# Kernel tuning notes

Measured on AMD Instinct MI355X. Metric: run time of the kernel, lower is better.

Reference implementation:

```python
import jax, jax.numpy as jnp
import numpy as np

EMBED_DIM = 1024
NUM_HEADS = 16
HEAD_DIM = EMBED_DIM // NUM_HEADS


def setup_inputs() -> dict:
    key = jax.random.key(0)
    ks = jax.random.split(key, 11)
    B, S, D = 2, 2048, EMBED_DIM
    s = 1.0 / np.sqrt(D)
    inp = {
        "query": jax.random.normal(ks[0], (B, S, D), jnp.float32),
        "key": jax.random.normal(ks[1], (B, S, D), jnp.float32),
        "value": jax.random.normal(ks[2], (B, S, D), jnp.float32),
        # torch Linear weights: [out, in]
        "Wq": jax.random.normal(ks[3], (D, D), jnp.float32) * s,
        "bq": jnp.zeros((D,), jnp.float32),
        "Wk": jax.random.normal(ks[4], (D, D), jnp.float32) * s,
        "bk": jnp.zeros((D,), jnp.float32),
        "Wv": jax.random.normal(ks[5], (D, D), jnp.float32) * s,
        "bv": jnp.zeros((D,), jnp.float32),
        "Wo": jax.random.normal(ks[6], (D, D), jnp.float32) * s,
        "bo": jnp.zeros((D,), jnp.float32),
    }
    return inp


def reference(query, key, value, Wq, bq, Wk, bk, Wv, bv, Wo, bo):
    B, Q, D = query.shape
    K = key.shape[1]
    H, Hd = NUM_HEADS, HEAD_DIM
    # NOTE: source divides by scaling = head_dim**-0.5, i.e. multiplies by sqrt(head_dim)
    scaling = float(Hd) ** (-0.5)

    q = (query @ Wq.T + bq).reshape(B, Q, H, Hd).transpose(0, 2, 1, 3)  # [B,H,Q,Hd]
    k = (key @ Wk.T + bk).reshape(B, K, H, Hd).transpose(0, 2, 1, 3)    # [B,H,K,Hd]
    v = (value @ Wv.T + bv).reshape(B, K, H, Hd).transpose(0, 2, 1, 3)  # [B,H,K,Hd]

    scores = jnp.einsum("bhqd,bhkd->bhqk", q, k) / scaling
    attn = jax.nn.softmax(scores, axis=-1)  # dropout=0 (eval)
    out = jnp.einsum("bhqk,bhkd->bhqd", attn, v)
    out = out.transpose(0, 2, 1, 3).reshape(B, Q, D)
    return out @ Wo.T + bo
```

## Files before the change

kernel.cpp:

```cpp
#include <hip/hip_runtime.h>
#include <type_traits>
#include <utility>

#define B_ 2
#define S_ 2048
#define D_ 1024
#define H_ 16
#define HD_ 64
#define KDIM 1024

typedef __attribute__((ext_vector_type(8))) short    s16x8;
typedef __attribute__((ext_vector_type(8))) _Float16 h16x8;
typedef __attribute__((ext_vector_type(4))) float    f32x4;
typedef __attribute__((ext_vector_type(4))) int      i32x4;
typedef __attribute__((ext_vector_type(2))) int      i32x2;

template <typename T, typename = void> struct mfma_takes : std::false_type {};
template <typename T>
struct mfma_takes<T, std::void_t<decltype(__builtin_amdgcn_mfma_f32_16x16x32_f16(
    std::declval<T>(), std::declval<T>(), std::declval<f32x4>(), 0, 0, 0))>>
    : std::true_type {};
using frag8 = std::conditional_t<mfma_takes<h16x8>::value, h16x8, s16x8>;

__device__ __forceinline__ f32x4 mfma_f16(frag8 a, frag8 b, f32x4 c) {
  return __builtin_amdgcn_mfma_f32_16x16x32_f16(a, b, c, 0, 0, 0);
}

__device__ __forceinline__ short f2h(float f) {
  _Float16 h = (_Float16)f;
  short s; __builtin_memcpy(&s, &h, 2);
  return s;
}
__device__ __forceinline__ int pk2h(float a, float b) {
  auto p = __builtin_amdgcn_cvt_pkrtz(a, b);
  int r; __builtin_memcpy(&r, &p, 4); return r;
}
__device__ __forceinline__ frag8 ld_frag(const short* p) {
  return __builtin_bit_cast(frag8, *(const i32x4*)p);
}
__device__ __forceinline__ float fast_exp2(float x) {
  return __builtin_amdgcn_exp2f(x);
}

typedef __attribute__((address_space(1))) const void gvoid;
typedef __attribute__((address_space(3))) void lvoid;
__device__ __forceinline__ void async_copy16(const void* g, void* l) {
  __builtin_amdgcn_global_load_lds((gvoid*)g, (lvoid*)l, 16, 0, 0);
}

#define RAW_BARRIER() asm volatile("s_barrier" ::: "memory")
#define WAITCNT_VM(n) asm volatile("s_waitcnt vmcnt(" #n ")" ::: "memory")

__global__ __launch_bounds__(256)
void conv_all(const float* __restrict__ q, const float* __restrict__ k,
              const float* __restrict__ v, const float* __restrict__ Wq,
              const float* __restrict__ Wk, const float* __restrict__ Wv,
              const float* __restrict__ Wo,
              short* __restrict__ qh, short* __restrict__ kh,
              short* __restrict__ vh, short* __restrict__ wq,
              short* __restrict__ wk, short* __restrict__ wv,
              short* __restrict__ wo) {
  const int blk = blockIdx.x;
  const float* src; short* dst; int base;
  if (blk < 2048)      { src = q;  dst = qh; base = blk; }
  else if (blk < 4096) { src = k;  dst = kh; base = blk - 2048; }
  else if (blk < 6144) { src = v;  dst = vh; base = blk - 4096; }
  else if (blk < 6656) { src = Wq; dst = wq; base = blk - 6144; }
  else if (blk < 7168) { src = Wk; dst = wk; base = blk - 6656; }
  else if (blk < 7680) { src = Wv; dst = wv; base = blk - 7168; }
  else                 { src = Wo; dst = wo; base = blk - 7680; }
  const int i = base * 2048 + threadIdx.x * 8;
  float4 a0 = *(const float4*)(src + i);
  float4 a1 = *(const float4*)(src + i + 4);
  short h[8] = { f2h(a0.x), f2h(a0.y), f2h(a0.z), f2h(a0.w),
                 f2h(a1.x), f2h(a1.y), f2h(a1.z), f2h(a1.w) };
  i32x4 ph; __builtin_memcpy(&ph, h, 16);
  *(i32x4*)(dst + i) = ph;
}

__global__ __launch_bounds__(256, 3)
void gemm_qkv(const short* __restrict__ qh, const short* __restrict__ kh,
              const short* __restrict__ vh, const short* __restrict__ wq,
              const short* __restrict__ wk, const short* __restrict__ wv,
              const float* __restrict__ bq, const float* __restrict__ bk,
              const float* __restrict__ bv, short* __restrict__ Qf,
              short* __restrict__ Kf, short* __restrict__ Vt, float QS) {
  __shared__ short As[3 * 4096];
  __shared__ short Bs[3 * 4096];

  const int blk = blockIdx.x;
  const int xcd = blk & 7, i = blk >> 3;
  const int p = (i >> 3) * 8 + xcd;
  const int bn = i & 7;
  const int z = p >> 5, bm = p & 31;
  const short* Ap = z == 0 ? qh : z == 1 ? kh : vh;
  const short* Wp = z == 0 ? wq : z == 1 ? wk : wv;
  const float* bias = z == 0 ? bq : z == 1 ? bk : bv;
  short* Out = z == 0 ? Qf : z == 1 ? Kf : Vt;
  const float scale = z == 0 ? QS : 1.0f;
  const int omode = z == 2 ? 2 : 1;

  const int t = threadIdx.x, wave = t >> 6, lane = t & 63;
  const int laneN = lane & 15, quad = lane >> 4;
  const int wm = wave & 1, wn = wave >> 1;

  f32x4 acc[4][4];
#pragma unroll
  for (int i2 = 0; i2 < 4; ++i2)
#pragma unroll
    for (int j = 0; j < 4; ++j)
#pragma unroll
      for (int r = 0; r < 4; ++r) acc[i2][j][r] = 0.f;

  auto stage = [&](int buf, int kk) {
#pragma unroll
    for (int j = 0; j < 2; ++j) {
      const int chunk = j * 256 + t;
      const int row = chunk >> 2;
      const int gg = (chunk & 3) ^ ((row >> 1) & 3);
      async_copy16(Ap + (size_t)(bm * 128 + row) * KDIM + kk + gg * 8,
                   As + buf * 4096 + chunk * 8);
      async_copy16(Wp + (size_t)(bn * 128 + row) * KDIM + kk + gg * 8,
                   Bs + buf * 4096 + chunk * 8);
    }
  };

  stage(0, 0);
  stage(1, 32);
  int buf = 0;
  for (int kk = 0; kk < KDIM; kk += 32) {
    if (kk + 64 < KDIM) {
      int nb = buf + 2; if (nb >= 3) nb -= 3;
      stage(nb, kk + 64);
      WAITCNT_VM(8);
    } else if (kk + 32 < KDIM) {
      WAITCNT_VM(4);
    } else {
      WAITCNT_VM(0);
    }
    RAW_BARRIER();

    frag8 aF[4], bF[4];
#pragma unroll
    for (int mi = 0; mi < 4; ++mi) {
      const int row = wm * 64 + mi * 16 + laneN;
      aF[mi] = ld_frag(As + buf * 4096 + row * 32 +
                       ((quad ^ ((row >> 1) & 3)) * 8));
    }
#pragma unroll
    for (int ni = 0; ni < 4; ++ni) {
      const int row = wn * 64 + ni * 16 + laneN;
      bF[ni] = ld_frag(Bs + buf * 4096 + row * 32 +
                       ((quad ^ ((row >> 1) & 3)) * 8));
    }
#pragma unroll
    for (int mi = 0; mi < 4; ++mi)
#pragma unroll
      for (int ni = 0; ni < 4; ++ni)
        acc[mi][ni] = mfma_f16(aF[mi], bF[ni], acc[mi][ni]);
    RAW_BARRIER();
    buf = buf + 1 == 3 ? 0 : buf + 1;
  }

  short* scr = As + wave * 1152;
  const int h = bn * 2 + wn;
  if (omode == 2) {
    const int bidx = bm >> 4;
    const int sbase = (bm * 128 + wm * 64) & 2047;
#pragma unroll
    for (int ni = 0; ni < 4; ++ni) {
      const float bb = bias[bn * 128 + wn * 64 + ni * 16 + laneN];
#pragma unroll
      for (int mi = 0; mi < 4; ++mi) {
        short pk[4];
#pragma unroll
        for (int r = 0; r < 4; ++r) pk[r] = f2h(acc[mi][ni][r] + bb);
        i32x2 w; __builtin_memcpy(&w, pk, 8);
        *(i32x2*)(scr + laneN * 72 + mi * 16 + quad * 4) = w;
      }
#pragma unroll
      for (int j = 0; j < 2; ++j) {
        const int ff = lane * 2 + j, hdr = ff >> 3, ch = ff & 7;
        i32x4 v = *(const i32x4*)(scr + hdr * 72 + ch * 8);
        *(i32x4*)(Vt + (((size_t)(bidx * H_ + h)) * HD_ + ni * 16 + hdr) * S_ +
                  sbase + ch * 8) = v;
      }
    }
  } else {
#pragma unroll
    for (int mi = 0; mi < 4; ++mi) {
#pragma unroll
      for (int ni = 0; ni < 4; ++ni) {
        const float bb = bias[bn * 128 + wn * 64 + ni * 16 + laneN];
#pragma unroll
        for (int r = 0; r < 4; ++r)
          scr[(quad * 4 + r) * 72 + ni * 16 + laneN] =
              f2h((acc[mi][ni][r] + bb) * scale);
      }
#pragma unroll
      for (int j = 0; j < 2; ++j) {
        const int ff = lane * 2 + j, row = ff >> 3, ch = ff & 7;
        const int rowg = bm * 128 + wm * 64 + mi * 16 + row;
        const int bidx = rowg >> 11, s = rowg & 2047;
        i32x4 v = *(const i32x4*)(scr + row * 72 + ch * 8);
        *(i32x4*)(Out + (((size_t)(bidx * H_ + h)) * S_ + s) * HD_ + ch * 8) = v;
      }
    }
  }
}

__global__ __launch_bounds__(256, 3)
void gemm_out(const short* __restrict__ Ap, const short* __restrict__ Wp,
              const float* __restrict__ bias, float* __restrict__ Out) {
  __shared__ short As[2 * 8192];
  __shared__ short Bs[2 * 4096];
  const int blk = blockIdx.x;
  const int xcd = blk & 7, i = blk >> 3;
  const int bm = (i >> 4) * 8 + xcd;
  const int bn = i & 15;

  const int t = threadIdx.x, wave = t >> 6, lane = t & 63;
  const int laneN = lane & 15, quad = lane >> 4;
  const int wm = wave & 1, wn = wave >> 1;

  f32x4 acc[4][2];
#pragma unroll
  for (int i2 = 0; i2 < 4; ++i2)
#pragma unroll
    for (int j = 0; j < 2; ++j)
#pragma unroll
      for (int r = 0; r < 4; ++r) acc[i2][j][r] = 0.f;

  auto stage = [&](int buf, int kk) {
#pragma unroll
    for (int j = 0; j < 4; ++j) {
      const int c = j * 256 + t;
      const int row = c >> 3, g = (c & 7) ^ (row & 7);
      async_copy16(Ap + (size_t)(bm * 128 + row) * KDIM + kk + g * 8,
                   As + buf * 8192 + c * 8);
    }
#pragma unroll
    for (int j = 0; j < 2; ++j) {
      const int c = j * 256 + t;
      const int row = c >> 3, g = (c & 7) ^ (row & 7);
      async_copy16(Wp + (size_t)(bn * 64 + row) * KDIM + kk + g * 8,
                   Bs + buf * 4096 + c * 8);
    }
  };

  int offA[4][2], offB[2][2];
#pragma unroll
  for (int mi = 0; mi < 4; ++mi) {
    const int row = wm * 64 + mi * 16 + laneN;
#pragma unroll
    for (int ks = 0; ks < 2; ++ks)
      offA[mi][ks] = row * 64 + (((quad + 4 * ks) ^ (row & 7)) * 8);
  }
#pragma unroll
  for (int ni = 0; ni < 2; ++ni) {
    const int row = wn * 32 + ni * 16 + laneN;
#pragma unroll
    for (int ks = 0; ks < 2; ++ks)
      offB[ni][ks] = row * 64 + (((quad + 4 * ks) ^ (row & 7)) * 8);
  }

  stage(0, 0);
  int buf = 0;
  for (int kk = 0; kk < KDIM; kk += 64) {
    if (kk + 64 < KDIM) {
      stage(buf ^ 1, kk + 64);
      WAITCNT_VM(6);
    } else {
      WAITCNT_VM(0);
    }
    RAW_BARRIER();

    frag8 aF[4][2], bF[2][2];
#pragma unroll
    for (int mi = 0; mi < 4; ++mi) {
      aF[mi][0] = ld_frag(As + buf * 8192 + offA[mi][0]);
      aF[mi][1] = ld_frag(As + buf * 8192 + offA[mi][1]);
    }
#pragma unroll
    for (int ni = 0; ni < 2; ++ni) {
      bF[ni][0] = ld_frag(Bs + buf * 4096 + offB[ni][0]);
      bF[ni][1] = ld_frag(Bs + buf * 4096 + offB[ni][1]);
    }
#pragma unroll
    for (int mi = 0; mi < 4; ++mi)
#pragma unroll
      for (int ni = 0; ni < 2; ++ni) {
        acc[mi][ni] = mfma_f16(aF[mi][0], bF[ni][0], acc[mi][ni]);
        acc[mi][ni] = mfma_f16(aF[mi][1], bF[ni][1], acc[mi][ni]);
      }
    RAW_BARRIER();
    buf ^= 1;
  }

  float* scr = (float*)As + wave * 576;
#pragma unroll
  for (int mi = 0; mi < 4; ++mi) {
#pragma unroll
    for (int ni = 0; ni < 2; ++ni) {
      const float bb = bias[bn * 64 + wn * 32 + ni * 16 + laneN];
#pragma unroll
      for (int r = 0; r < 4; ++r)
        scr[(quad * 4 + r) * 36 + ni * 16 + laneN] = acc[mi][ni][r] + bb;
    }
#pragma unroll
    for (int j = 0; j < 2; ++j) {
      const int ff = lane * 2 + j, row = ff >> 3, ch = ff & 7;
      const int rowg = bm * 128 + wm * 64 + mi * 16 + row;
      f32x4 v = *(const f32x4*)(scr + row * 36 + ch * 4);
      *(f32x4*)(Out + (size_t)rowg * 1024 + bn * 64 + wn * 32 + ch * 4) = v;
    }
  }
}

__global__ __launch_bounds__(512, 4)
void attn(const short* __restrict__ Qf, const short* __restrict__ Kf,
          const short* __restrict__ Vt_, short* __restrict__ Ow) {
  __shared__ short Ks[4 * 4096];
  __shared__ short Vts[4 * 4096];
  __shared__ short Ps[8][16 * 64];

  const int blk = blockIdx.x;
  const int xcd = blk & 7, local = blk >> 3;
  const int pair = xcd * 4 + (local >> 4);
  const int h = pair & 15, b = pair >> 4, qt = local & 15;
  const size_t head = ((size_t)b * H_ + h) * (size_t)S_ * HD_;

  const int t = threadIdx.x;
  const int wave = t >> 6, lane = t & 63;
  const int laneN = lane & 15, quad = lane >> 4;

  frag8 qf[2];
  {
    const size_t row = (size_t)qt * 128 + wave * 16 + laneN;
#pragma unroll
    for (int half = 0; half < 2; ++half)
      qf[half] = ld_frag(Qf + head + row * HD_ + half * 32 + quad * 8);
  }

  f32x4 o[4];
  float m_r = -1e30f, l_r = 0.f;
#pragma unroll
  for (int i = 0; i < 4; ++i)
#pragma unroll
    for (int j = 0; j < 4; ++j) o[i][j] = 0.f;

  const int srow = t >> 3, sg = (t & 7) ^ (srow & 7);
  const short* kp = Kf + head + (size_t)srow * HD_ + sg * 8;
  const short* vp = Vt_ + head + (size_t)srow * S_ + sg * 8;
  const int d = t * 8;

  int off[4][2];
#pragma unroll
  for (int nt = 0; nt < 4; ++nt) {
    const int row = nt * 16 + laneN;
    off[nt][0] = row * 64 + ((quad ^ (row & 7)) * 8);
    off[nt][1] = row * 64 + (((quad + 4) ^ (row & 7)) * 8);
  }

  short* const pwr = &Ps[wave][0] + laneN * 64;
  short* pw[4];
#pragma unroll
  for (int nt = 0; nt < 4; ++nt) {
    const int g = nt * 2 + (quad >> 1);
    pw[nt] = pwr + ((g + laneN) & 7) * 8 + (quad & 1) * 4;
  }
  const short* prd0 = pwr + ((quad + laneN) & 7) * 8;
  const short* prd1 = pwr + (((quad + 4) + laneN) & 7) * 8;

  async_copy16(kp, Ks + d);  async_copy16(vp, Vts + d);
  kp += 4096; vp += 64;
  async_copy16(kp, Ks + 4096 + d);  async_copy16(vp, Vts + 4096 + d);
  kp += 4096; vp += 64;

  f32x4 s[4];
  WAITCNT_VM(2);
  RAW_BARRIER();
  {
    __builtin_amdgcn_s_setprio(1);
#pragma unroll
    for (int nt = 0; nt < 4; ++nt) {
      frag8 k0 = ld_frag(Ks + off[nt][0]);
      frag8 k1 = ld_frag(Ks + off[nt][1]);
      f32x4 acc = {0.f, 0.f, 0.f, 0.f};
      acc = mfma_f16(k0, qf[0], acc);
      acc = mfma_f16(k1, qf[1], acc);
      s[nt] = acc;
    }
    __builtin_amdgcn_s_setprio(0);
  }

#define ATTN_TILE(B0, STG, QKN)                                              \
  {                                                                          \
    if (STG == 1) {                                                          \
      async_copy16(kp, Ks + (((B0) + 2) & 3) * 4096 + d);                    \
      async_copy16(vp, Vts + (((B0) + 2) & 3) * 4096 + d);                   \
      kp += 4096; vp += 64;                                                  \
      WAITCNT_VM(2);                                                         \
    } else if (STG == 2) {                                                   \
      WAITCNT_VM(0);                                                         \
    }                                                                        \
    RAW_BARRIER();                                                           \
    const short* VbS = Vts + (B0) * 4096;                                    \
                              \
    frag8 vf[4][2];                                                          \
    _Pragma("unroll")                                                        \
    for (int dt = 0; dt < 4; ++dt) {                                         \
      vf[dt][0] = ld_frag(VbS + off[dt][0]);                                 \
      vf[dt][1] = ld_frag(VbS + off[dt][1]);                                 \
    }                                                                        \
                         \
    f32x4 sn[4];                                                             \
    if (QKN) {                                                               \
      const short* KbS = Ks + (((B0) + 1) & 3) * 4096;                       \
      __builtin_amdgcn_s_setprio(1);                                         \
      _Pragma("unroll")                                                      \
      for (int nt = 0; nt < 4; ++nt) {                                       \
        frag8 k0 = ld_frag(KbS + off[nt][0]);                                \
        frag8 k1 = ld_frag(KbS + off[nt][1]);                                \
        f32x4 acc = {0.f, 0.f, 0.f, 0.f};                                    \
        acc = mfma_f16(k0, qf[0], acc);                                      \
        acc = mfma_f16(k1, qf[1], acc);                                      \
        sn[nt] = acc;                                                        \
      }                                                                      \
      __builtin_amdgcn_s_setprio(0);                                         \
    }                                                                        \
             \
    {                                                                        \
      float mt[4];                                                           \
      _Pragma("unroll")                                                      \
      for (int nt = 0; nt < 4; ++nt)                                         \
        mt[nt] = fmaxf(fmaxf(s[nt][0], s[nt][1]),                            \
                       fmaxf(s[nt][2], s[nt][3]));                           \
      float mx = fmaxf(fmaxf(mt[0], mt[1]), fmaxf(mt[2], mt[3]));            \
      mx = fmaxf(mx, __shfl_xor(mx, 16));                                    \
      mx = fmaxf(mx, __shfl_xor(mx, 32));                                    \
      if (__any(mx > m_r + 8.f)) {         \
        const float mn = fmaxf(m_r, mx);                                     \
        const float al = fast_exp2(m_r - mn);                                \
        m_r = mn;                                                            \
        l_r *= al;                                                           \
        _Pragma("unroll")                                                    \
        for (int dt = 0; dt < 4; ++dt)                                       \
          _Pragma("unroll")                                                  \
          for (int r = 0; r < 4; ++r) o[dt][r] *= al;                        \
      }                                                                      \
      float rt[4];                                                           \
      _Pragma("unroll")                                                      \
      for (int nt = 0; nt < 4; ++nt) {                                       \
        const float p0 = fast_exp2(s[nt][0] - m_r);                          \
        const float p1 = fast_exp2(s[nt][1] - m_r);                          \
        const float p2 = fast_exp2(s[nt][2] - m_r);                          \
        const float p3 = fast_exp2(s[nt][3] - m_r);                          \
        s[nt][0] = p0; s[nt][1] = p1; s[nt][2] = p2; s[nt][3] = p3;          \
        rt[nt] = (p0 + p1) + (p2 + p3);                                      \
      }                                                                      \
      float rs = (rt[0] + rt[1]) + (rt[2] + rt[3]);                          \
      rs += __shfl_xor(rs, 16);                                              \
      rs += __shfl_xor(rs, 32);                                              \
      l_r += rs;                                                             \
    }                                                                        \
            \
    _Pragma("unroll")                                                        \
    for (int nt = 0; nt < 4; ++nt) {                                         \
      i32x2 w;                                                               \
      w[0] = pk2h(s[nt][0], s[nt][1]);                                       \
      w[1] = pk2h(s[nt][2], s[nt][3]);                                       \
      *(i32x2*)pw[nt] = w;                                                   \
    }                                                                        \
          \
    const frag8 p0 = ld_frag(prd0);                                          \
    const frag8 p1 = ld_frag(prd1);                                          \
    __builtin_amdgcn_s_setprio(1);                                           \
    _Pragma("unroll")                                                        \
    for (int dt = 0; dt < 4; ++dt) {                                         \
      o[dt] = mfma_f16(vf[dt][0], p0, o[dt]);                                \
      o[dt] = mfma_f16(vf[dt][1], p1, o[dt]);                                \
    }                                                                        \
    __builtin_amdgcn_s_setprio(0);                                           \
    if (QKN) {                                                               \
      _Pragma("unroll")                                                      \
      for (int nt = 0; nt < 4; ++nt) s[nt] = sn[nt];                         \
    }                                                                        \
  }

  for (int it = 0; it < 7; ++it) {
    ATTN_TILE(0, 1, 1)
    ATTN_TILE(1, 1, 1)
    ATTN_TILE(2, 1, 1)
    ATTN_TILE(3, 1, 1)
  }
  ATTN_TILE(0, 1, 1)
  ATTN_TILE(1, 1, 1)
  ATTN_TILE(2, 2, 1)
  ATTN_TILE(3, 0, 0)
#undef ATTN_TILE

  {
    const float inv = 1.0f / l_r;
    const int sgq = qt * 128 + wave * 16 + laneN;
    short* dst = Ow + ((size_t)b * S_ + sgq) * D_ + h * HD_;
#pragma unroll
    for (int dt = 0; dt < 4; ++dt) {
      short pk[4] = { f2h(o[dt][0] * inv), f2h(o[dt][1] * inv),
                      f2h(o[dt][2] * inv), f2h(o[dt][3] * inv) };
      i32x2 w; __builtin_memcpy(&w, pk, 8);
      *(i32x2*)(dst + dt * 16 + quad * 4) = w;
    }
  }
}

extern "C" void kernel_launch(void* const* d_in, const int* in_sizes, int n_in,
                              void* d_out, int out_size, void* d_ws, size_t ws_size,
                              hipStream_t stream) {
  const float* q  = (const float*)d_in[0];
  const float* k  = (const float*)d_in[1];
  const float* v  = (const float*)d_in[2];
  const float* Wq = (const float*)d_in[3];
  const float* bq = (const float*)d_in[4];
  const float* Wk = (const float*)d_in[5];
  const float* bk = (const float*)d_in[6];
  const float* Wv = (const float*)d_in[7];
  const float* bv = (const float*)d_in[8];
  const float* Wo = (const float*)d_in[9];
  const float* bo = (const float*)d_in[10];

  const size_t NTOK = (size_t)B_ * S_ * D_;
  const size_t NW   = (size_t)D_ * D_;
  short* p = (short*)d_ws;
  short* qh = p; p += NTOK;  short* kh = p; p += NTOK;  short* vh = p; p += NTOK;
  short* wq = p; p += NW;    short* wk = p; p += NW;
  short* wv = p; p += NW;    short* wo = p; p += NW;
  short* Qf = p; p += NTOK;  short* Kf = p; p += NTOK;
  short* Vt = p; p += NTOK;  short* Ow = p; p += NTOK;

  dim3 blk(256);

  conv_all<<<8192, blk, 0, stream>>>(q, k, v, Wq, Wk, Wv, Wo,
                                     qh, kh, vh, wq, wk, wv, wo);

  const float QS = 11.541560327111707f;
  gemm_qkv<<<768, blk, 0, stream>>>(qh, kh, vh, wq, wk, wv, bq, bk, bv,
                                    Qf, Kf, Vt, QS);

  attn<<<512, dim3(512), 0, stream>>>(Qf, Kf, Vt, Ow);

  gemm_out<<<512, blk, 0, stream>>>(Ow, wo, bo, (float*)d_out);
}
```

Baseline: 225.1 us.

## Rewrite attention with 32x32 MFMA, register-resident P via permlane32 swap

The attention kernel moves from 16x16x32 MFMA tiles (8 waves, 16 query rows each) to 32x32x16 MFMA tiles (4 waves, 32 query rows each). The P matrix no longer goes through LDS: it is repacked in registers with v_permlane32_swap and fed straight into the PV MFMA. The lookahead QK computation for the next tile is dropped. The larger tiles should halve K/V LDS reads per FLOP and remove the P round-trip, at the cost of more registers per wave, fewer waves per block, and less overlap between softmax and MFMA.

```diff
diff --git a/kernel.cpp b/kernel.cpp
--- a/kernel.cpp
+++ b/kernel.cpp
@@ -12,6 +12,7 @@
 typedef __attribute__((ext_vector_type(8))) short    s16x8;
 typedef __attribute__((ext_vector_type(8))) _Float16 h16x8;
 typedef __attribute__((ext_vector_type(4))) float    f32x4;
+typedef __attribute__((ext_vector_type(16))) float   f32x16;
 typedef __attribute__((ext_vector_type(4))) int      i32x4;
 typedef __attribute__((ext_vector_type(2))) int      i32x2;
 
@@ -25,6 +26,9 @@
 __device__ __forceinline__ f32x4 mfma_f16(frag8 a, frag8 b, f32x4 c) {
   return __builtin_amdgcn_mfma_f32_16x16x32_f16(a, b, c, 0, 0, 0);
 }
+__device__ __forceinline__ f32x16 mfma32(frag8 a, frag8 b, f32x16 c) {
+  return __builtin_amdgcn_mfma_f32_32x32x16_f16(a, b, c, 0, 0, 0);
+}
 
 __device__ __forceinline__ short f2h(float f) {
   _Float16 h = (_Float16)f;
@@ -40,6 +44,9 @@
 }
 __device__ __forceinline__ float fast_exp2(float x) {
   return __builtin_amdgcn_exp2f(x);
+}
+__device__ __forceinline__ void pl32swap(int& a, int& b) {
+  asm volatile("v_permlane32_swap_b32 %0, %1" : "+v"(a), "+v"(b));
 }
 
 typedef __attribute__((address_space(1))) const void gvoid;
@@ -317,12 +324,11 @@
   }
 }
 
-__global__ __launch_bounds__(512, 4)
+__global__ __launch_bounds__(256, 2)
 void attn(const short* __restrict__ Qf, const short* __restrict__ Kf,
           const short* __restrict__ Vt_, short* __restrict__ Ow) {
   __shared__ short Ks[4 * 4096];
   __shared__ short Vts[4 * 4096];
-  __shared__ short Ps[8][16 * 64];
 
   const int blk = blockIdx.x;
   const int xcd = blk & 7, local = blk >> 3;
@@ -332,184 +338,170 @@
 
   const int t = threadIdx.x;
   const int wave = t >> 6, lane = t & 63;
-  const int laneN = lane & 15, quad = lane >> 4;
-
-  frag8 qf[2];
+  const int l31 = lane & 31, hi = lane >> 5;
+
+  const int q0 = qt * 128 + wave * 32;
+
+  frag8 qf[4];
   {
-    const size_t row = (size_t)qt * 128 + wave * 16 + laneN;
-#pragma unroll
-    for (int half = 0; half < 2; ++half)
-      qf[half] = ld_frag(Qf + head + row * HD_ + half * 32 + quad * 8);
-  }
-
-  f32x4 o[4];
+    const short* qp = Qf + head + (size_t)(q0 + l31) * HD_ + hi * 8;
+#pragma unroll
+    for (int ds = 0; ds < 4; ++ds) qf[ds] = ld_frag(qp + ds * 16);
+  }
+
+  f32x16 o0, o1;
+#pragma unroll
+  for (int r = 0; r < 16; ++r) { o0[r] = 0.f; o1[r] = 0.f; }
   float m_r = -1e30f, l_r = 0.f;
-#pragma unroll
-  for (int i = 0; i < 4; ++i)
-#pragma unroll
-    for (int j = 0; j < 4; ++j) o[i][j] = 0.f;
-
-  const int srow = t >> 3, sg = (t & 7) ^ (srow & 7);
-  const short* kp = Kf + head + (size_t)srow * HD_ + sg * 8;
-  const short* vp = Vt_ + head + (size_t)srow * S_ + sg * 8;
-  const int d = t * 8;
-
-  int off[4][2];
-#pragma unroll
-  for (int nt = 0; nt < 4; ++nt) {
-    const int row = nt * 16 + laneN;
-    off[nt][0] = row * 64 + ((quad ^ (row & 7)) * 8);
-    off[nt][1] = row * 64 + (((quad + 4) ^ (row & 7)) * 8);
-  }
-
-  short* const pwr = &Ps[wave][0] + laneN * 64;
-  short* pw[4];
-#pragma unroll
-  for (int nt = 0; nt < 4; ++nt) {
-    const int g = nt * 2 + (quad >> 1);
-    pw[nt] = pwr + ((g + laneN) & 7) * 8 + (quad & 1) * 4;
-  }
-  const short* prd0 = pwr + ((quad + laneN) & 7) * 8;
-  const short* prd1 = pwr + (((quad + 4) + laneN) & 7) * 8;
-
-  async_copy16(kp, Ks + d);  async_copy16(vp, Vts + d);
-  kp += 4096; vp += 64;
-  async_copy16(kp, Ks + 4096 + d);  async_copy16(vp, Vts + 4096 + d);
-  kp += 4096; vp += 64;
-
-  f32x4 s[4];
-  WAITCNT_VM(2);
-  RAW_BARRIER();
-  {
-    __builtin_amdgcn_s_setprio(1);
-#pragma unroll
-    for (int nt = 0; nt < 4; ++nt) {
-      frag8 k0 = ld_frag(Ks + off[nt][0]);
-      frag8 k1 = ld_frag(Ks + off[nt][1]);
-      f32x4 acc = {0.f, 0.f, 0.f, 0.f};
-      acc = mfma_f16(k0, qf[0], acc);
-      acc = mfma_f16(k1, qf[1], acc);
-      s[nt] = acc;
-    }
-    __builtin_amdgcn_s_setprio(0);
-  }
-
-#define ATTN_TILE(B0, STG, QKN)                                              \
+
+  const int c0 = t, c1 = 256 + t;
+  const int r0 = c0 >> 3, gg0 = (c0 & 7) ^ (r0 & 7);
+  const int r1 = c1 >> 3, gg1 = (c1 & 7) ^ (r1 & 7);
+  const short* kp0 = Kf + head + (size_t)r0 * HD_ + gg0 * 8;
+  const short* kp1 = Kf + head + (size_t)r1 * HD_ + gg1 * 8;
+  const short* vp0 = Vt_ + head + (size_t)r0 * S_ + gg0 * 8;
+  const short* vp1 = Vt_ + head + (size_t)r1 * S_ + gg1 * 8;
+  const int d0 = c0 * 8, d1 = c1 * 8;
+
+  int off2[2][4];
+#pragma unroll
+  for (int hf = 0; hf < 2; ++hf) {
+    const int row = hf * 32 + l31;
+#pragma unroll
+    for (int j = 0; j < 4; ++j)
+      off2[hf][j] = row * 64 + (((j * 2 + hi) ^ (row & 7)) * 8);
+  }
+
+  async_copy16(kp0, Ks + d0);  async_copy16(kp1, Ks + d1);
+  async_copy16(vp0, Vts + d0); async_copy16(vp1, Vts + d1);
+  kp0 += 4096; kp1 += 4096; vp0 += 64; vp1 += 64;
+  async_copy16(kp0, Ks + 4096 + d0);  async_copy16(kp1, Ks + 4096 + d1);
+  async_copy16(vp0, Vts + 4096 + d0); async_copy16(vp1, Vts + 4096 + d1);
+  kp0 += 4096; kp1 += 4096; vp0 += 64; vp1 += 64;
+
+#define ATTN_TILE(B0, STG)                                                   \
   {                                                                          \
     if (STG == 1) {                                                          \
-      async_copy16(kp, Ks + (((B0) + 2) & 3) * 4096 + d);                    \
-      async_copy16(vp, Vts + (((B0) + 2) & 3) * 4096 + d);                   \
-      kp += 4096; vp += 64;                                                  \
-      WAITCNT_VM(2);                                                         \
+      const int nb = ((B0) + 2) & 3;                                         \
+      async_copy16(kp0, Ks + nb * 4096 + d0);                                \
+      async_copy16(kp1, Ks + nb * 4096 + d1);                                \
+      async_copy16(vp0, Vts + nb * 4096 + d0);                               \
+      async_copy16(vp1, Vts + nb * 4096 + d1);                               \
+      kp0 += 4096; kp1 += 4096; vp0 += 64; vp1 += 64;                        \
+      WAITCNT_VM(8);                                                         \
     } else if (STG == 2) {                                                   \
+      WAITCNT_VM(4);                                                         \
+    } else {                                                                 \
       WAITCNT_VM(0);                                                         \
     }                                                                        \
     RAW_BARRIER();                                                           \
+    const short* KbS = Ks + (B0) * 4096;                                     \
     const short* VbS = Vts + (B0) * 4096;                                    \
-                              \
-    frag8 vf[4][2];                                                          \
+                  \
+    f32x16 sA, sB;                                                           \
     _Pragma("unroll")                                                        \
-    for (int dt = 0; dt < 4; ++dt) {                                         \
-      vf[dt][0] = ld_frag(VbS + off[dt][0]);                                 \
-      vf[dt][1] = ld_frag(VbS + off[dt][1]);                                 \
+    for (int r = 0; r < 16; ++r) { sA[r] = 0.f; sB[r] = 0.f; }               \
+    __builtin_amdgcn_s_setprio(1);                                           \
+    _Pragma("unroll")                                                        \
+    for (int ds = 0; ds < 4; ++ds) {                                         \
+      frag8 ka = ld_frag(KbS + off2[0][ds]);                                 \
+      frag8 kb = ld_frag(KbS + off2[1][ds]);                                 \
+      sA = mfma32(ka, qf[ds], sA);                                           \
+      sB = mfma32(kb, qf[ds], sB);                                           \
     }                                                                        \
-                         \
-    f32x4 sn[4];                                                             \
-    if (QKN) {                                                               \
-      const short* KbS = Ks + (((B0) + 1) & 3) * 4096;                       \
-      __builtin_amdgcn_s_setprio(1);                                         \
+    __builtin_amdgcn_s_setprio(0);                                           \
+                 \
+    {                                                                        \
+      float mA = sA[0], mB = sB[0];                                          \
       _Pragma("unroll")                                                      \
-      for (int nt = 0; nt < 4; ++nt) {                                       \
-        frag8 k0 = ld_frag(KbS + off[nt][0]);                                \
-        frag8 k1 = ld_frag(KbS + off[nt][1]);                                \
-        f32x4 acc = {0.f, 0.f, 0.f, 0.f};                                    \
-        acc = mfma_f16(k0, qf[0], acc);                                      \
-        acc = mfma_f16(k1, qf[1], acc);                                      \
-        sn[nt] = acc;                                                        \
+      for (int r = 1; r < 16; ++r) {                                         \
+        mA = fmaxf(mA, sA[r]); mB = fmaxf(mB, sB[r]);                        \
       }                                                                      \
-      __builtin_amdgcn_s_setprio(0);                                         \
-    }                                                                        \
-             \
-    {                                                                        \
-      float mt[4];                                                           \
-      _Pragma("unroll")                                                      \
-      for (int nt = 0; nt < 4; ++nt)                                         \
-        mt[nt] = fmaxf(fmaxf(s[nt][0], s[nt][1]),                            \
-                       fmaxf(s[nt][2], s[nt][3]));                           \
-      float mx = fmaxf(fmaxf(mt[0], mt[1]), fmaxf(mt[2], mt[3]));            \
-      mx = fmaxf(mx, __shfl_xor(mx, 16));                                    \
+      float mx = fmaxf(mA, mB);                                              \
       mx = fmaxf(mx, __shfl_xor(mx, 32));                                    \
-      if (__any(mx > m_r + 8.f)) {         \
+      if (__any(mx > m_r + 8.f)) {                                           \
         const float mn = fmaxf(m_r, mx);                                     \
         const float al = fast_exp2(m_r - mn);                                \
-        m_r = mn;                                                            \
-        l_r *= al;                                                           \
+        m_r = mn; l_r *= al;                                                 \
         _Pragma("unroll")                                                    \
-        for (int dt = 0; dt < 4; ++dt)                                       \
-          _Pragma("unroll")                                                  \
-          for (int r = 0; r < 4; ++r) o[dt][r] *= al;                        \
+        for (int r = 0; r < 16; ++r) { o0[r] *= al; o1[r] *= al; }           \
       }                                                                      \
-      float rt[4];                                                           \
+      float rs = 0.f;                                                        \
       _Pragma("unroll")                                                      \
-      for (int nt = 0; nt < 4; ++nt) {                                       \
-        const float p0 = fast_exp2(s[nt][0] - m_r);                          \
-        const float p1 = fast_exp2(s[nt][1] - m_r);                          \
-        const float p2 = fast_exp2(s[nt][2] - m_r);                          \
-        const float p3 = fast_exp2(s[nt][3] - m_r);                          \
-        s[nt][0] = p0; s[nt][1] = p1; s[nt][2] = p2; s[nt][3] = p3;          \
-        rt[nt] = (p0 + p1) + (p2 + p3);                                      \
+      for (int r = 0; r < 16; ++r) {                                         \
+        const float pa = fast_exp2(sA[r] - m_r);                             \
+        const float pb = fast_exp2(sB[r] - m_r);                             \
+        sA[r] = pa; sB[r] = pb; rs += pa + pb;                               \
       }                                                                      \
-      float rs = (rt[0] + rt[1]) + (rt[2] + rt[3]);                          \
-      rs += __shfl_xor(rs, 16);                                              \
       rs += __shfl_xor(rs, 32);                                              \
       l_r += rs;                                                             \
     }                                                                        \
-            \
-    _Pragma("unroll")                                                        \
-    for (int nt = 0; nt < 4; ++nt) {                                         \
-      i32x2 w;                                                               \
-      w[0] = pk2h(s[nt][0], s[nt][1]);                                       \
-      w[1] = pk2h(s[nt][2], s[nt][3]);                                       \
-      *(i32x2*)pw[nt] = w;                                                   \
+       \
+    frag8 pf0, pf1, pf2, pf3;                                                \
+    {                                                                        \
+      int w0, w1, w2, w3; i32x4 fw;                                          \
+      w0 = pk2h(sA[0], sA[1]);   w1 = pk2h(sA[2], sA[3]);                    \
+      w2 = pk2h(sA[4], sA[5]);   w3 = pk2h(sA[6], sA[7]);                    \
+      pl32swap(w0, w2); pl32swap(w1, w3);                                    \
+      fw[0] = w0; fw[1] = w1; fw[2] = w2; fw[3] = w3;                        \
+      pf0 = __builtin_bit_cast(frag8, fw);                                   \
+      w0 = pk2h(sA[8], sA[9]);   w1 = pk2h(sA[10], sA[11]);                  \
+      w2 = pk2h(sA[12], sA[13]); w3 = pk2h(sA[14], sA[15]);                  \
+      pl32swap(w0, w2); pl32swap(w1, w3);                                    \
+      fw[0] = w0; fw[1] = w1; fw[2] = w2; fw[3] = w3;                        \
+      pf1 = __builtin_bit_cast(frag8, fw);                                   \
+      w0 = pk2h(sB[0], sB[1]);   w1 = pk2h(sB[2], sB[3]);                    \
+      w2 = pk2h(sB[4], sB[5]);   w3 = pk2h(sB[6], sB[7]);                    \
+      pl32swap(w0, w2); pl32swap(w1, w3);                                    \
+      fw[0] = w0; fw[1] = w1; fw[2] = w2; fw[3] = w3;                        \
+      pf2 = __builtin_bit_cast(frag8, fw);                                   \
+      w0 = pk2h(sB[8], sB[9]);   w1 = pk2h(sB[10], sB[11]);                  \
+      w2 = pk2h(sB[12], sB[13]); w3 = pk2h(sB[14], sB[15]);                  \
+      pl32swap(w0, w2); pl32swap(w1, w3);                                    \
+      fw[0] = w0; fw[1] = w1; fw[2] = w2; fw[3] = w3;                        \
+      pf3 = __builtin_bit_cast(frag8, fw);                                   \
     }                                                                        \
-          \
-    const frag8 p0 = ld_frag(prd0);                                          \
-    const frag8 p1 = ld_frag(prd1);                                          \
+                        \
     __builtin_amdgcn_s_setprio(1);                                           \
-    _Pragma("unroll")                                                        \
-    for (int dt = 0; dt < 4; ++dt) {                                         \
-      o[dt] = mfma_f16(vf[dt][0], p0, o[dt]);                                \
-      o[dt] = mfma_f16(vf[dt][1], p1, o[dt]);                                \
+    {                                                                        \
+      frag8 va, vb;                                                          \
+      va = ld_frag(VbS + off2[0][0]); o0 = mfma32(va, pf0, o0);              \
+      vb = ld_frag(VbS + off2[1][0]); o1 = mfma32(vb, pf0, o1);              \
+      va = ld_frag(VbS + off2[0][1]); o0 = mfma32(va, pf1, o0);              \
+      vb = ld_frag(VbS + off2[1][1]); o1 = mfma32(vb, pf1, o1);              \
+      va = ld_frag(VbS + off2[0][2]); o0 = mfma32(va, pf2, o0);              \
+      vb = ld_frag(VbS + off2[1][2]); o1 = mfma32(vb, pf2, o1);              \
+      va = ld_frag(VbS + off2[0][3]); o0 = mfma32(va, pf3, o0);              \
+      vb = ld_frag(VbS + off2[1][3]); o1 = mfma32(vb, pf3, o1);              \
     }                                                                        \
     __builtin_amdgcn_s_setprio(0);                                           \
-    if (QKN) {                                                               \
-      _Pragma("unroll")                                                      \
-      for (int nt = 0; nt < 4; ++nt) s[nt] = sn[nt];                         \
-    }                                                                        \
   }
 
   for (int it = 0; it < 7; ++it) {
-    ATTN_TILE(0, 1, 1)
-    ATTN_TILE(1, 1, 1)
-    ATTN_TILE(2, 1, 1)
-    ATTN_TILE(3, 1, 1)
-  }
-  ATTN_TILE(0, 1, 1)
-  ATTN_TILE(1, 1, 1)
-  ATTN_TILE(2, 2, 1)
-  ATTN_TILE(3, 0, 0)
+    ATTN_TILE(0, 1)
+    ATTN_TILE(1, 1)
+    ATTN_TILE(2, 1)
+    ATTN_TILE(3, 1)
+  }
+  ATTN_TILE(0, 1)
+  ATTN_TILE(1, 1)
+  ATTN_TILE(2, 2)
+  ATTN_TILE(3, 0)
 #undef ATTN_TILE
 
   {
     const float inv = 1.0f / l_r;
-    const int sgq = qt * 128 + wave * 16 + laneN;
-    short* dst = Ow + ((size_t)b * S_ + sgq) * D_ + h * HD_;
-#pragma unroll
-    for (int dt = 0; dt < 4; ++dt) {
-      short pk[4] = { f2h(o[dt][0] * inv), f2h(o[dt][1] * inv),
-                      f2h(o[dt][2] * inv), f2h(o[dt][3] * inv) };
-      i32x2 w; __builtin_memcpy(&w, pk, 8);
-      *(i32x2*)(dst + dt * 16 + quad * 4) = w;
+    short* dst = Ow + ((size_t)b * S_ + q0 + l31) * D_ + h * HD_ + hi * 4;
+#pragma unroll
+    for (int rg = 0; rg < 4; ++rg) {
+      i32x2 w;
+      w[0] = pk2h(o0[rg * 4 + 0] * inv, o0[rg * 4 + 1] * inv);
+      w[1] = pk2h(o0[rg * 4 + 2] * inv, o0[rg * 4 + 3] * inv);
+      *(i32x2*)(dst + rg * 8) = w;
+      i32x2 w2;
+      w2[0] = pk2h(o1[rg * 4 + 0] * inv, o1[rg * 4 + 1] * inv);
+      w2[1] = pk2h(o1[rg * 4 + 2] * inv, o1[rg * 4 + 3] * inv);
+      *(i32x2*)(dst + 32 + rg * 8) = w2;
     }
   }
 }
@@ -547,7 +539,7 @@
   gemm_qkv<<<768, blk, 0, stream>>>(qh, kh, vh, wq, wk, wv, bq, bk, bv,
                                     Qf, Kf, Vt, QS);
 
-  attn<<<512, dim3(512), 0, stream>>>(Qf, Kf, Vt, Ow);
+  attn<<<512, dim3(256), 0, stream>>>(Qf, Kf, Vt, Ow);
 
   gemm_out<<<512, blk, 0, stream>>>(Ow, wo, bo, (float*)d_out);
 }
```

Result: no change. 222.4 us (-1.2%).
